# Kernel optimization log

Measured on AMD Instinct MI355X. Metric: run time of the kernel, lower is better.

The kernel has to match this reference:

```python
import jax, jax.numpy as jnp
import numpy as np
from jax import lax

EPS = 1e-5      # InstanceNorm2d default eps
SLOPE = 0.2     # LeakyReLU negative slope
K = 3           # kernel size
PAD = 1


def _conv(x, w, pad=PAD):
    # x: [B,C,H,W], w: [O,I,K,K], stride 1
    return lax.conv_general_dilated(x, w, (1, 1), [(pad, pad), (pad, pad)],
                                    dimension_numbers=('NCHW', 'OIHW', 'NCHW'))


def _instance_norm(x, gamma, beta):
    mu = jnp.mean(x, (2, 3), keepdims=True)
    var = jnp.mean((x - mu) ** 2, (2, 3), keepdims=True)
    xn = (x - mu) * lax.rsqrt(var + EPS)
    return xn * gamma[None, :, None, None] + beta[None, :, None, None]


def _lrelu(x):
    return jnp.where(x >= 0, x, SLOPE * x)


def _deform_conv(x, w_off, b_off, w_def):
    # DCNv2: offsets+mask predicted by a 3x3 conv, then modulated bilinear sampling.
    B, C, H, W = x.shape
    om = _conv(x, w_off) + b_off[None, :, None, None]       # [B, 3*K*K, H, W]
    o1, o2, m = jnp.split(om, 3, axis=1)                    # each [B, K*K, H, W]
    off = jnp.concatenate([o1, o2], axis=1)                 # [B, 2*K*K, H, W]
    dy = off[:, 0::2]                                       # [B, K*K, H, W] y-offsets
    dx = off[:, 1::2]                                       # [B, K*K, H, W] x-offsets
    mask = jax.nn.sigmoid(m)                                # [B, K*K, H, W]

    ky = jnp.repeat(jnp.arange(K), K).astype(x.dtype)       # tap row index per k
    kx = jnp.tile(jnp.arange(K), K).astype(x.dtype)         # tap col index per k
    py = dy + jnp.arange(H, dtype=x.dtype)[None, None, :, None] - PAD + ky[None, :, None, None]
    px = dx + jnp.arange(W, dtype=x.dtype)[None, None, None, :] - PAD + kx[None, :, None, None]

    y0 = jnp.floor(py); x0 = jnp.floor(px)
    ly = py - y0; lx = px - x0
    y0i = y0.astype(jnp.int32); x0i = x0.astype(jnp.int32)

    xf = x.reshape(B, C, H * W)

    def gather(iy, ix):
        valid = ((iy >= 0) & (iy < H) & (ix >= 0) & (ix < W)).astype(x.dtype)
        idx = jnp.clip(iy, 0, H - 1) * W + jnp.clip(ix, 0, W - 1)
        v = jax.vmap(lambda f, i: jnp.take(f, i, axis=-1))(xf, idx)  # [B,C,K*K,H,W]
        return v * valid[:, None]

    samp = (gather(y0i, x0i)         * ((1 - ly) * (1 - lx))[:, None]
          + gather(y0i, x0i + 1)     * ((1 - ly) * lx)[:, None]
          + gather(y0i + 1, x0i)     * (ly * (1 - lx))[:, None]
          + gather(y0i + 1, x0i + 1) * (ly * lx)[:, None])          # [B,C,K*K,H,W]

    wk = w_def.reshape(w_def.shape[0], C, K * K)            # [O,C,K*K]
    return jnp.einsum('ock,bckhw,bkhw->bohw', wk, samp, mask)


def setup_inputs() -> dict:
    key = jax.random.key(0)
    ks = jax.random.split(key, 10)
    B, C, H, W = 4, 128, 96, 96
    x = jax.random.normal(ks[0], (B, C, H, W), jnp.float32)
    g1 = 1.0 + 0.05 * jax.random.normal(ks[1], (C,), jnp.float32)
    b1 = 0.05 * jax.random.normal(ks[2], (C,), jnp.float32)
    g2 = 1.0 + 0.05 * jax.random.normal(ks[3], (C,), jnp.float32)
    b2 = 0.05 * jax.random.normal(ks[4], (C,), jnp.float32)
    w1 = jax.random.normal(ks[5], (C, C, K, K), jnp.float32) * 0.03
    bc1 = 0.01 * jax.random.normal(ks[6], (C,), jnp.float32)
    # offset/mask conv: zero-init in the original; use small random values so the
    # irregular bilinear-sampling path is actually exercised.
    w_off = jax.random.normal(ks[7], (3 * K * K, C, K, K), jnp.float32) * 0.01
    b_off = 0.01 * jax.random.normal(ks[8], (3 * K * K,), jnp.float32)
    w_def = jax.random.normal(ks[9], (C, C, K, K), jnp.float32) * 0.03  # DeformConv has bias=None
    return {"x": x, "g1": g1, "b1": b1, "g2": g2, "b2": b2,
            "w1": w1, "bc1": bc1, "w_off": w_off, "b_off": b_off, "w_def": w_def}


def reference(x, g1, b1, g2, b2, w1, bc1, w_off, b_off, w_def):
    h = _lrelu(_instance_norm(x, g1, b1))
    h = _conv(h, w1) + bc1[None, :, None, None]
    h = _lrelu(_instance_norm(h, g2, b2))
    h = _deform_conv(h, w_off, b_off, w_def)
    return h + x
```

## Files before the change

### kernel.cpp

```cpp
#include <hip/hip_runtime.h>
#include <hip/hip_fp16.h>
#include <math.h>

#define HWN 9216
#define HD 96
#define WD 96

typedef _Float16 h8v __attribute__((ext_vector_type(8)));
typedef float f16x16 __attribute__((ext_vector_type(16)));

__device__ __forceinline__ ushort f2h(float f) {
  return __half_as_ushort(__float2half(f));
}
__device__ __forceinline__ __half2 u2h(unsigned u) {
  return __builtin_bit_cast(__half2, u);
}
__device__ __forceinline__ unsigned h2u(__half2 h) {
  return __builtin_bit_cast(unsigned, h);
}
__device__ __forceinline__ h8v u4h(uint4 v) {
  return __builtin_bit_cast(h8v, v);
}
__device__ __forceinline__ f16x16 mfma32(h8v a, h8v b, f16x16 c) {
  return __builtin_amdgcn_mfma_f32_32x32x16_f16(a, b, c, 0, 0, 0);
}
__device__ __forceinline__ __half2 pkmax2(__half2 a, __half2 b) {
  unsigned r;
  asm("v_pk_max_f16 %0, %1, %2" : "=v"(r) : "v"(h2u(a)), "v"(h2u(b)));
  return u2h(r);
}
__device__ __forceinline__ __half2 lrelu2(__half2 v, __half2 c02) {
  return pkmax2(v, __hmul2(v, c02));
}

__global__ __launch_bounds__(256) void packxt_kernel(
    const float* __restrict__ w1, const float* __restrict__ wdef,
    const float* __restrict__ woff, const float* __restrict__ x,
    ushort* __restrict__ w1p, ushort* __restrict__ wdp, ushort* __restrict__ wofp,
    unsigned* __restrict__ xh, float* __restrict__ partS, float* __restrict__ partQ) {
  __shared__ float tl[128][97];
  int bid = blockIdx.x;
  int t = threadIdx.x;
  if (bid < 162) {
    int i = bid * 256 + t;
    const float* src;
    ushort* dst;
    int CT, CO_real, fi;
    if (i < 18432) { src = w1; dst = w1p; CT = 4; CO_real = 128; fi = i; }
    else if (i < 36864) { src = wdef; dst = wdp; CT = 4; CO_real = 128; fi = i - 18432; }
    else { src = woff; dst = wofp; CT = 1; CO_real = 27; fi = i - 36864; }
    int lane = fi & 63;
    int j = fi >> 6;
    int ks = j & 7; j >>= 3;
    int ct = j % CT;
    int kk = j / CT;
    int co = ct * 32 + (lane & 31);
    int c0 = ks * 16 + (lane >> 5) * 8;
    ushort fr[8];
#pragma unroll
    for (int e = 0; e < 8; ++e) {
      float v = 0.f;
      if (co < CO_real) v = src[(size_t)(co * 128 + c0 + e) * 9 + kk];
      fr[e] = f2h(v);
    }
    uint4 o4;
    o4.x = (unsigned)fr[0] | ((unsigned)fr[1] << 16);
    o4.y = (unsigned)fr[2] | ((unsigned)fr[3] << 16);
    o4.z = (unsigned)fr[4] | ((unsigned)fr[5] << 16);
    o4.w = (unsigned)fr[6] | ((unsigned)fr[7] << 16);
    *(uint4*)(dst + (size_t)fi * 8) = o4;
    return;
  }
  int xb = bid - 162;
  int b = xb / 96, y = xb % 96;
  const float* sbase = x + (size_t)b * 128 * HWN + y * WD;
  for (int i = t; i < 12288; i += 256) {
    int c = i / 96, xx = i - c * 96;
    tl[c][xx] = sbase[(size_t)c * HWN + xx];
  }
  __syncthreads();
  {
    int c = t >> 1, half = t & 1;
    float S = 0.f, Q = 0.f;
    for (int j = 0; j < 48; ++j) {
      float v = tl[c][half * 48 + j];
      S += v;
      Q += v * v;
    }
    S += __shfl_xor(S, 1, 64);
    Q += __shfl_xor(Q, 1, 64);
    if (half == 0) {
      partS[((size_t)(b * 96 + y)) * 128 + c] = S;
      partQ[((size_t)(b * 96 + y)) * 128 + c] = Q;
    }
  }
  unsigned* dbase = xh + (size_t)(b * 96 + y) * 96 * 64;
  for (int i = t; i < 6144; i += 256) {
    int xx = i >> 6, c2 = i & 63;
    unsigned lo = f2h(tl[2 * c2][xx]);
    unsigned hi = f2h(tl[2 * c2 + 1][xx]);
    dbase[xx * 64 + c2] = lo | (hi << 16);
  }
}

__global__ __launch_bounds__(64) void finalize_kernel(
    const float* __restrict__ partS, const float* __restrict__ partQ,
    const float* __restrict__ gamma, const float* __restrict__ beta,
    float* __restrict__ sa_, float* __restrict__ sb_, int ntiles) {
  int bc = blockIdx.x;
  int b = bc >> 7, c = bc & 127;
  float S = 0.f, Q = 0.f;
  for (int tl = threadIdx.x; tl < ntiles; tl += 64) {
    S += partS[((size_t)b * ntiles + tl) * 128 + c];
    Q += partQ[((size_t)b * ntiles + tl) * 128 + c];
  }
#pragma unroll
  for (int off = 32; off > 0; off >>= 1) {
    S += __shfl_down(S, off, 64);
    Q += __shfl_down(Q, off, 64);
  }
  if (threadIdx.x == 0) {
    float mu = S / (float)HWN;
    float var = Q / (float)HWN - mu * mu;
    float rs = rsqrtf(var + 1e-5f);
    float a = rs * gamma[c];
    sa_[bc] = a;
    sb_[bc] = beta[c] - mu * a;
  }
}

__global__ __launch_bounds__(256) void stats2_kernel(
    const ushort* __restrict__ hBh, float* __restrict__ partS,
    float* __restrict__ partQ) {
  int tile = blockIdx.x;
  int b = blockIdx.y;
  int t = threadIdx.x;
  int cc = t & 15, pp = t >> 4;
  int wid = t >> 6, lane = t & 63;
  const ushort* base = hBh + ((size_t)b * HWN + tile * 144) * 128 + cc * 8;
  float S[8], Q[8];
#pragma unroll
  for (int e = 0; e < 8; ++e) { S[e] = 0.f; Q[e] = 0.f; }
  for (int i = 0; i < 9; ++i) {
    int pix = i * 16 + pp;
    uint4 v = *(const uint4*)(base + (size_t)pix * 128);
    unsigned ar[4] = {v.x, v.y, v.z, v.w};
#pragma unroll
    for (int j = 0; j < 4; ++j) {
      float2 f = __half22float2(u2h(ar[j]));
      S[2 * j] += f.x; Q[2 * j] += f.x * f.x;
      S[2 * j + 1] += f.y; Q[2 * j + 1] += f.y * f.y;
    }
  }
#pragma unroll
  for (int e = 0; e < 8; ++e) {
    S[e] += __shfl_xor(S[e], 16, 64); Q[e] += __shfl_xor(Q[e], 16, 64);
    S[e] += __shfl_xor(S[e], 32, 64); Q[e] += __shfl_xor(Q[e], 32, 64);
  }
  __shared__ float red[2][4][16][8];
  if (lane < 16) {
#pragma unroll
    for (int e = 0; e < 8; ++e) { red[0][wid][lane][e] = S[e]; red[1][wid][lane][e] = Q[e]; }
  }
  __syncthreads();
  if (t < 16) {
#pragma unroll
    for (int e = 0; e < 8; ++e) {
      float s = red[0][0][t][e] + red[0][1][t][e] + red[0][2][t][e] + red[0][3][t][e];
      float q = red[1][0][t][e] + red[1][1][t][e] + red[1][2][t][e] + red[1][3][t][e];
      partS[((size_t)b * 64 + tile) * 128 + t * 8 + e] = s;
      partQ[((size_t)b * 64 + tile) * 128 + t * 8 + e] = q;
    }
  }
}

__global__ __launch_bounds__(512) void conv1_mfma(
    const ushort* __restrict__ inp, const float* __restrict__ sa_,
    const float* __restrict__ sb_, const ushort* __restrict__ wp,
    const float* __restrict__ bias, ushort* __restrict__ outh) {
  __shared__ ushort halo[100 * 128];
  __shared__ __half2 sah[64], sbh[64];
  int b = blockIdx.y;
  int tile = blockIdx.x;
  int Y0 = (tile / 12) * 8, X0 = (tile % 12) * 8;
  int t = threadIdx.x;
  int lane = t & 63, w = t >> 6;
  if (t < 64) {
    sah[t] = __floats2half2_rn(sa_[b * 128 + 2 * t], sa_[b * 128 + 2 * t + 1]);
    sbh[t] = __floats2half2_rn(sb_[b * 128 + 2 * t], sb_[b * 128 + 2 * t + 1]);
  }
  __syncthreads();
  const __half2 c02 = __float2half2_rn(0.2f);
  const ushort* ib = inp + (size_t)b * HWN * 128;
  for (int i = t; i < 400; i += 512) {
    int r = i >> 2, q = i & 3;
    int gy = Y0 - 1 + r / 10, gx = X0 - 1 + r % 10;
    bool inb = ((unsigned)gy < 96u) && ((unsigned)gx < 96u);
    const uint4* gp4 = (const uint4*)(ib + (size_t)(gy * 96 + gx) * 128 + q * 32);
#pragma unroll
    for (int cc = 0; cc < 4; ++cc) {
      uint4 v = make_uint4(0, 0, 0, 0);
      if (inb) {
        uint4 g = gp4[cc];
        unsigned ar[4] = {g.x, g.y, g.z, g.w};
        int c2b = (q * 4 + cc) * 4;
#pragma unroll
        for (int j = 0; j < 4; ++j) {
          __half2 hv = __hfma2(u2h(ar[j]), sah[c2b + j], sbh[c2b + j]);
          hv = lrelu2(hv, c02);
          ar[j] = h2u(hv);
        }
        v.x = ar[0]; v.y = ar[1]; v.z = ar[2]; v.w = ar[3];
      }
      int ch = (q * 4 + cc) ^ (r & 7);
      *(uint4*)&halo[r * 128 + ch * 8] = v;
    }
  }
  __syncthreads();

  int ct = w >> 1, pt = w & 1;
  int pl = lane & 31, kh = lane >> 5;
  int p = pt * 32 + pl;
  f16x16 acc = (f16x16)(0.f);

  uint4 Acur[8], Anxt[8];
#pragma unroll
  for (int ks = 0; ks < 8; ++ks)
    Acur[ks] = *(const uint4*)(wp + (size_t)((0 * 4 + ct) * 8 + ks) * 512 + lane * 8);

  for (int kk = 0; kk < 9; ++kk) {
    if (kk < 8) {
#pragma unroll
      for (int ks = 0; ks < 8; ++ks)
        Anxt[ks] = *(const uint4*)(wp + (size_t)(((kk + 1) * 4 + ct) * 8 + ks) * 512 + lane * 8);
    }
    int ky = kk / 3, kx = kk % 3;
    int r = ((p >> 3) + ky) * 10 + (p & 7) + kx;
    __builtin_amdgcn_s_setprio(1);
#pragma unroll
    for (int ks = 0; ks < 8; ++ks) {
      int u = (ks * 2 + kh) ^ (r & 7);
      h8v bf = *(const h8v*)&halo[r * 128 + u * 8];
      acc = mfma32(u4h(Acur[ks]), bf, acc);
    }
    __builtin_amdgcn_s_setprio(0);
    if (kk < 8) {
#pragma unroll
      for (int ks = 0; ks < 8; ++ks) Acur[ks] = Anxt[ks];
    }
  }
  int gp = (Y0 + (p >> 3)) * 96 + X0 + (p & 7);
#pragma unroll
  for (int g = 0; g < 4; ++g) {
    int ch0 = ct * 32 + 4 * kh + 8 * g;
    float v0 = acc[4 * g + 0] + bias[ch0 + 0];
    float v1 = acc[4 * g + 1] + bias[ch0 + 1];
    float v2 = acc[4 * g + 2] + bias[ch0 + 2];
    float v3 = acc[4 * g + 3] + bias[ch0 + 3];
    uint2 o;
    o.x = (unsigned)f2h(v0) | ((unsigned)f2h(v1) << 16);
    o.y = (unsigned)f2h(v2) | ((unsigned)f2h(v3) << 16);
    *(uint2*)&outh[((size_t)b * HWN + gp) * 128 + ch0] = o;
  }
}

__device__ __forceinline__ uint4 gaffine(const ushort* hb, int pix, int cc,
                                         const __half2* sa2v, const __half2* sb2v,
                                         __half2 c02) {
  uint4 g = *(const uint4*)(hb + (size_t)pix * 128 + cc * 8);
  unsigned ar[4] = {g.x, g.y, g.z, g.w};
#pragma unroll
  for (int j = 0; j < 4; ++j) {
    __half2 hv = __hfma2(u2h(ar[j]), sa2v[j], sb2v[j]);
    hv = lrelu2(hv, c02);
    ar[j] = h2u(hv);
  }
  return make_uint4(ar[0], ar[1], ar[2], ar[3]);
}

__global__ __launch_bounds__(256) void deform_fused(
    const ushort* __restrict__ h2n, const float* __restrict__ sa_,
    const float* __restrict__ sb_, const ushort* __restrict__ wofp,
    const float* __restrict__ boff, const ushort* __restrict__ wdp,
    const float* __restrict__ x, float* __restrict__ out) {
  __shared__ __align__(16) ushort halo[96 * 128];
  __shared__ __align__(16) ushort S[2][32 * 128];
  __shared__ __align__(16) ushort4 idxs[9][32];
  __shared__ __align__(16) ushort4 wgtc[9][32];
  __shared__ __half2 sah[64], sbh[64];
  float* pf = (float*)S;
  int bid = blockIdx.x;
  int swz = (bid & 7) * 144 + (bid >> 3);
  int b = swz / 288;
  int tile = swz % 288;
  int Y0 = (tile / 12) * 4, X0 = (tile % 12) * 8;
  int t = threadIdx.x;
  int lane = t & 63, w = t >> 6;
  const ushort* hb = h2n + (size_t)b * HWN * 128;
  if (t < 64) {
    sah[t] = __floats2half2_rn(sa_[b * 128 + 2 * t], sa_[b * 128 + 2 * t + 1]);
    sbh[t] = __floats2half2_rn(sb_[b * 128 + 2 * t], sb_[b * 128 + 2 * t + 1]);
  }
  __syncthreads();
  const __half2 c02 = __float2half2_rn(0.2f);

  for (int i = t; i < 1536; i += 256) {
    int pix = i >> 4, u = i & 15;
    int gy = Y0 - 2 + pix / 12, gx = X0 - 2 + pix % 12;
    uint4 v = make_uint4(0, 0, 0, 0);
    if (((unsigned)gy < 96u) && ((unsigned)gx < 96u)) {
      uint4 g = *(const uint4*)(hb + (size_t)(gy * 96 + gx) * 128 + u * 8);
      unsigned ar[4] = {g.x, g.y, g.z, g.w};
#pragma unroll
      for (int j = 0; j < 4; ++j) {
        __half2 hv = __hfma2(u2h(ar[j]), sah[u * 4 + j], sbh[u * 4 + j]);
        hv = lrelu2(hv, c02);
        ar[j] = h2u(hv);
      }
      v.x = ar[0]; v.y = ar[1]; v.z = ar[2]; v.w = ar[3];
    }
    *(uint4*)&halo[pix * 128 + ((u ^ (pix & 15)) * 8)] = v;
  }
  __syncthreads();

  {
    int pl = lane & 31, kh = lane >> 5;
    int p = pl;
    f16x16 accm = (f16x16)(0.f);
    for (int kk = w; kk < 9; kk += 4) {
      int ky = kk / 3, kx = kk % 3;
      int hp = (1 + (p >> 3) + ky) * 12 + 1 + (p & 7) + kx;
#pragma unroll
      for (int ks = 0; ks < 8; ++ks) {
        uint4 a = *(const uint4*)(wofp + (size_t)(kk * 8 + ks) * 512 + lane * 8);
        int u = (ks * 2 + kh) ^ (hp & 15);
        h8v bf = *(const h8v*)&halo[hp * 128 + u * 8];
        accm = mfma32(u4h(a), bf, accm);
      }
    }
#pragma unroll
    for (int reg = 0; reg < 16; ++reg) {
      int co = 4 * kh + (reg & 3) + 8 * (reg >> 2);
      pf[(w * 32 + co) * 32 + p] = accm[reg];
    }
  }
  __syncthreads();

  for (int i = t; i < 288; i += 256) {
    int k = i >> 5, p = i & 31;
    int yy = Y0 + (p >> 3), xx = X0 + (p & 7);
    int cdy = 2 * k, cdx = 2 * k + 1, cm = 18 + k;
    float dy = pf[(0 * 32 + cdy) * 32 + p] + pf[(1 * 32 + cdy) * 32 + p] +
               pf[(2 * 32 + cdy) * 32 + p] + pf[(3 * 32 + cdy) * 32 + p] + boff[cdy];
    float dx = pf[(0 * 32 + cdx) * 32 + p] + pf[(1 * 32 + cdx) * 32 + p] +
               pf[(2 * 32 + cdx) * 32 + p] + pf[(3 * 32 + cdx) * 32 + p] + boff[cdx];
    float mv = pf[(0 * 32 + cm) * 32 + p] + pf[(1 * 32 + cm) * 32 + p] +
               pf[(2 * 32 + cm) * 32 + p] + pf[(3 * 32 + cm) * 32 + p] + boff[cm];
    float mask = 1.0f / (1.0f + expf(-mv));
    float py = dy + (float)(yy - 1 + (k / 3));
    float px = dx + (float)(xx - 1 + (k % 3));
    float fy = floorf(py), fx = floorf(px);
    float lyf = py - fy, lxf = px - fx;
    int y0 = (int)fy, x0 = (int)fx;
    int y1 = y0 + 1, x1 = x0 + 1;
    bool vy0 = (y0 >= 0) && (y0 < HD);
    bool vy1 = (y1 >= 0) && (y1 < HD);
    bool vx0 = (x0 >= 0) && (x0 < WD);
    bool vx1 = (x1 >= 0) && (x1 < WD);
    int y0c = min(max(y0, 0), HD - 1), y1c = min(max(y1, 0), HD - 1);
    int x0c = min(max(x0, 0), WD - 1), x1c = min(max(x1, 0), WD - 1);
    float w0 = (1.f - lyf) * (1.f - lxf) * ((vy0 && vx0) ? mask : 0.f);
    float w1v = (1.f - lyf) * lxf * ((vy0 && vx1) ? mask : 0.f);
    float w2 = lyf * (1.f - lxf) * ((vy1 && vx0) ? mask : 0.f);
    float w3 = lyf * lxf * ((vy1 && vx1) ? mask : 0.f);
    bool inh = (y0c >= Y0 - 2) && (y1c <= Y0 + 5) && (x0c >= X0 - 2) && (x1c <= X0 + 9);
    ushort4 sidx;
    if (inh) {
      int sy0 = y0c - (Y0 - 2), sy1 = y1c - (Y0 - 2);
      int sx0 = x0c - (X0 - 2), sx1 = x1c - (X0 - 2);
      sidx.x = (ushort)(sy0 * 12 + sx0);
      sidx.y = (ushort)(sy0 * 12 + sx1);
      sidx.z = (ushort)(sy1 * 12 + sx0);
      sidx.w = (ushort)(sy1 * 12 + sx1);
    } else {
      sidx.x = (ushort)((y0c * WD + x0c) | 0x8000);
      sidx.y = (ushort)(y0c * WD + x1c);
      sidx.z = (ushort)(y1c * WD + x0c);
      sidx.w = (ushort)(y1c * WD + x1c);
    }
    idxs[k][p] = sidx;
    ushort4 wc;
    wc.x = f2h(w0); wc.y = f2h(w1v); wc.z = f2h(w2); wc.w = f2h(w3);
    wgtc[k][p] = wc;
  }
  __syncthreads();

  int cc = t & 15;
  int pp = t >> 4;
  int ct = w;
  int pl = lane & 31, kh = lane >> 5;
  int pg = pl;
  f16x16 acc = (f16x16)(0.f);
  __half2 sa2v[4], sb2v[4];
#pragma unroll
  for (int j = 0; j < 4; ++j) { sa2v[j] = sah[cc * 4 + j]; sb2v[j] = sbh[cc * 4 + j]; }

  int gp = (Y0 + (pg >> 3)) * 96 + X0 + (pg & 7);
  float xr[16];
#pragma unroll
  for (int reg = 0; reg < 16; ++reg) {
    int co = ct * 32 + 4 * kh + (reg & 3) + 8 * (reg >> 2);
    xr[reg] = x[(size_t)(b * 128 + co) * HWN + gp];
  }

  uint4 AW[8];
  for (int k = 0; k < 9; ++k) {
    const ushort* wk = wdp + (size_t)k * 16384;
#pragma unroll
    for (int ks = 0; ks < 8; ++ks)
      AW[ks] = *(const uint4*)(wk + (size_t)(ct * 8 + ks) * 512 + lane * 8);
    ushort* Sb_w = S[k & 1];
#pragma unroll
    for (int i2 = 0; i2 < 2; ++i2) {
      int p = pp + 16 * i2;
      ushort4 sidx = idxs[k][p];
      ushort4 wc = wgtc[k][p];
      uint4 C0, C1, C2, C3;
      if (sidx.x & 0x8000u) {
        C0 = gaffine(hb, sidx.x & 0x7fff, cc, sa2v, sb2v, c02);
        C1 = gaffine(hb, sidx.y, cc, sa2v, sb2v, c02);
        C2 = gaffine(hb, sidx.z, cc, sa2v, sb2v, c02);
        C3 = gaffine(hb, sidx.w, cc, sa2v, sb2v, c02);
      } else {
        C0 = *(const uint4*)&halo[sidx.x * 128 + ((cc ^ (sidx.x & 15)) * 8)];
        C1 = *(const uint4*)&halo[sidx.y * 128 + ((cc ^ (sidx.y & 15)) * 8)];
        C2 = *(const uint4*)&halo[sidx.z * 128 + ((cc ^ (sidx.z & 15)) * 8)];
        C3 = *(const uint4*)&halo[sidx.w * 128 + ((cc ^ (sidx.w & 15)) * 8)];
      }
      __half2 a0 = u2h((unsigned)wc.x * 0x10001u);
      __half2 a1 = u2h((unsigned)wc.y * 0x10001u);
      __half2 a2 = u2h((unsigned)wc.z * 0x10001u);
      __half2 a3 = u2h((unsigned)wc.w * 0x10001u);
      __half2 s0 = __hmul2(u2h(C0.x), a0);
      __half2 s1 = __hmul2(u2h(C0.y), a0);
      __half2 s2 = __hmul2(u2h(C0.z), a0);
      __half2 s3 = __hmul2(u2h(C0.w), a0);
      s0 = __hfma2(u2h(C1.x), a1, s0); s1 = __hfma2(u2h(C1.y), a1, s1);
      s2 = __hfma2(u2h(C1.z), a1, s2); s3 = __hfma2(u2h(C1.w), a1, s3);
      s0 = __hfma2(u2h(C2.x), a2, s0); s1 = __hfma2(u2h(C2.y), a2, s1);
      s2 = __hfma2(u2h(C2.z), a2, s2); s3 = __hfma2(u2h(C2.w), a2, s3);
      s0 = __hfma2(u2h(C3.x), a3, s0); s1 = __hfma2(u2h(C3.y), a3, s1);
      s2 = __hfma2(u2h(C3.z), a3, s2); s3 = __hfma2(u2h(C3.w), a3, s3);
      uint4 o4;
      o4.x = h2u(s0); o4.y = h2u(s1); o4.z = h2u(s2); o4.w = h2u(s3);
      *(uint4*)&Sb_w[p * 128 + ((cc ^ (p & 15)) * 8)] = o4;
    }
    asm volatile("s_waitcnt lgkmcnt(0)" ::: "memory");
    __builtin_amdgcn_s_barrier();
    const ushort* Sb = S[k & 1];
    __builtin_amdgcn_s_setprio(1);
#pragma unroll
    for (int ks = 0; ks < 8; ++ks) {
      int u = (ks * 2 + kh) ^ (pg & 15);
      h8v bf = *(const h8v*)&Sb[pg * 128 + u * 8];
      acc = mfma32(u4h(AW[ks]), bf, acc);
    }
    __builtin_amdgcn_s_setprio(0);
  }
#pragma unroll
  for (int reg = 0; reg < 16; ++reg) {
    int co = ct * 32 + 4 * kh + (reg & 3) + 8 * (reg >> 2);
    size_t oi = (size_t)(b * 128 + co) * HWN + gp;
    out[oi] = acc[reg] + xr[reg];
  }
}

extern "C" void kernel_launch(void* const* d_in, const int* in_sizes, int n_in,
                              void* d_out, int out_size, void* d_ws, size_t ws_size,
                              hipStream_t stream) {
  const float* x = (const float*)d_in[0];
  const float* g1 = (const float*)d_in[1];
  const float* b1 = (const float*)d_in[2];
  const float* g2 = (const float*)d_in[3];
  const float* b2 = (const float*)d_in[4];
  const float* w1 = (const float*)d_in[5];
  const float* bc1 = (const float*)d_in[6];
  const float* w_off = (const float*)d_in[7];
  const float* b_off = (const float*)d_in[8];
  const float* w_def = (const float*)d_in[9];
  float* out = (float*)d_out;
  float* ws = (float*)d_ws;

  ushort* w1p = (ushort*)ws;
  ushort* wofp = (ushort*)(ws + 73728);
  ushort* wdp = (ushort*)(ws + 92160);
  float* sa1 = ws + 165888;
  float* sb1 = ws + 166400;
  float* sa2 = ws + 166912;
  float* sb2 = ws + 167424;
  float* partS1 = ws + 167936;
  float* partQ1 = ws + 217088;
  float* partS2 = ws + 266240;
  float* partQ2 = ws + 299008;
  ushort* xh = (ushort*)(ws + 331776);
  ushort* hBh = (ushort*)(ws + 2691072);

  packxt_kernel<<<546, 256, 0, stream>>>(w1, w_def, w_off, x, w1p, wdp, wofp,
                                         (unsigned*)xh, partS1, partQ1);
  finalize_kernel<<<512, 64, 0, stream>>>(partS1, partQ1, g1, b1, sa1, sb1, 96);
  conv1_mfma<<<dim3(144, 4), 512, 0, stream>>>(xh, sa1, sb1, w1p, bc1, hBh);
  stats2_kernel<<<dim3(64, 4), 256, 0, stream>>>(hBh, partS2, partQ2);
  finalize_kernel<<<512, 64, 0, stream>>>(partS2, partQ2, g2, b2, sa2, sb2, 64);
  deform_fused<<<dim3(1152), 256, 0, stream>>>(hBh, sa2, sb2, wofp, b_off, wdp, x, out);
}
```

Before: 81.90 us.

## Fold instance-norm finalize into consumer kernels and vectorize x tile loads

Removes the two finalize_kernel launches by having each block of conv1_mfma and deform_fused reduce the per-tile partial sums itself and compute the norm scale and shift in shared memory. Also switches the x-tile load in packxt to float4 reads. This cuts two kernel launches and their dependency gaps. In exchange every block redundantly re-reads the partial sums (96 or 64 rows by 128 channels, twice) and pays extra barriers at kernel start.

```diff
diff --git a/kernel.cpp b/kernel.cpp
--- a/kernel.cpp
+++ b/kernel.cpp
@@ -74,9 +74,13 @@
   int xb = bid - 162;
   int b = xb / 96, y = xb % 96;
   const float* sbase = x + (size_t)b * 128 * HWN + y * WD;
-  for (int i = t; i < 12288; i += 256) {
-    int c = i / 96, xx = i - c * 96;
-    tl[c][xx] = sbase[(size_t)c * HWN + xx];
+  for (int i = t; i < 3072; i += 256) {
+    int c = i / 24, j = i - c * 24;
+    const float4 v = *(const float4*)(sbase + (size_t)c * HWN + j * 4);
+    tl[c][j * 4 + 0] = v.x;
+    tl[c][j * 4 + 1] = v.y;
+    tl[c][j * 4 + 2] = v.z;
+    tl[c][j * 4 + 3] = v.w;
   }
   __syncthreads();
   {
@@ -100,32 +104,6 @@
     unsigned lo = f2h(tl[2 * c2][xx]);
     unsigned hi = f2h(tl[2 * c2 + 1][xx]);
     dbase[xx * 64 + c2] = lo | (hi << 16);
-  }
-}
-
-__global__ __launch_bounds__(64) void finalize_kernel(
-    const float* __restrict__ partS, const float* __restrict__ partQ,
-    const float* __restrict__ gamma, const float* __restrict__ beta,
-    float* __restrict__ sa_, float* __restrict__ sb_, int ntiles) {
-  int bc = blockIdx.x;
-  int b = bc >> 7, c = bc & 127;
-  float S = 0.f, Q = 0.f;
-  for (int tl = threadIdx.x; tl < ntiles; tl += 64) {
-    S += partS[((size_t)b * ntiles + tl) * 128 + c];
-    Q += partQ[((size_t)b * ntiles + tl) * 128 + c];
-  }
-#pragma unroll
-  for (int off = 32; off > 0; off >>= 1) {
-    S += __shfl_down(S, off, 64);
-    Q += __shfl_down(Q, off, 64);
-  }
-  if (threadIdx.x == 0) {
-    float mu = S / (float)HWN;
-    float var = Q / (float)HWN - mu * mu;
-    float rs = rsqrtf(var + 1e-5f);
-    float a = rs * gamma[c];
-    sa_[bc] = a;
-    sb_[bc] = beta[c] - mu * a;
   }
 }
 
@@ -175,8 +153,9 @@
 }
 
 __global__ __launch_bounds__(512) void conv1_mfma(
-    const ushort* __restrict__ inp, const float* __restrict__ sa_,
-    const float* __restrict__ sb_, const ushort* __restrict__ wp,
+    const ushort* __restrict__ inp, const float* __restrict__ partS1,
+    const float* __restrict__ partQ1, const float* __restrict__ g1v,
+    const float* __restrict__ b1v, const ushort* __restrict__ wp,
     const float* __restrict__ bias, ushort* __restrict__ outh) {
   __shared__ ushort halo[100 * 128];
   __shared__ __half2 sah[64], sbh[64];
@@ -185,9 +164,34 @@
   int Y0 = (tile / 12) * 8, X0 = (tile % 12) * 8;
   int t = threadIdx.x;
   int lane = t & 63, w = t >> 6;
+  float* fredp = (float*)halo;
+  float* saf = fredp + 1024;
+  float* sbf = saf + 128;
+  {
+    int c = t & 127, g = t >> 7;
+    float S = 0.f, Q = 0.f;
+    for (int r = g * 24; r < g * 24 + 24; ++r) {
+      S += partS1[((size_t)(b * 96 + r)) * 128 + c];
+      Q += partQ1[((size_t)(b * 96 + r)) * 128 + c];
+    }
+    fredp[(0 * 4 + g) * 128 + c] = S;
+    fredp[(1 * 4 + g) * 128 + c] = Q;
+  }
+  __syncthreads();
+  if (t < 128) {
+    float S = fredp[0 * 128 + t] + fredp[1 * 128 + t] + fredp[2 * 128 + t] + fredp[3 * 128 + t];
+    float Q = fredp[4 * 128 + t] + fredp[5 * 128 + t] + fredp[6 * 128 + t] + fredp[7 * 128 + t];
+    float mu = S / (float)HWN;
+    float var = Q / (float)HWN - mu * mu;
+    float rs = rsqrtf(var + 1e-5f);
+    float a = rs * g1v[t];
+    saf[t] = a;
+    sbf[t] = b1v[t] - mu * a;
+  }
+  __syncthreads();
   if (t < 64) {
-    sah[t] = __floats2half2_rn(sa_[b * 128 + 2 * t], sa_[b * 128 + 2 * t + 1]);
-    sbh[t] = __floats2half2_rn(sb_[b * 128 + 2 * t], sb_[b * 128 + 2 * t + 1]);
+    sah[t] = __floats2half2_rn(saf[2 * t], saf[2 * t + 1]);
+    sbh[t] = __floats2half2_rn(sbf[2 * t], sbf[2 * t + 1]);
   }
   __syncthreads();
   const __half2 c02 = __float2half2_rn(0.2f);
@@ -279,8 +283,9 @@
 }
 
 __global__ __launch_bounds__(256) void deform_fused(
-    const ushort* __restrict__ h2n, const float* __restrict__ sa_,
-    const float* __restrict__ sb_, const ushort* __restrict__ wofp,
+    const ushort* __restrict__ h2n, const float* __restrict__ partS2,
+    const float* __restrict__ partQ2, const float* __restrict__ g2v,
+    const float* __restrict__ b2v, const ushort* __restrict__ wofp,
     const float* __restrict__ boff, const ushort* __restrict__ wdp,
     const float* __restrict__ x, float* __restrict__ out) {
   __shared__ __align__(16) ushort halo[96 * 128];
@@ -297,11 +302,38 @@
   int t = threadIdx.x;
   int lane = t & 63, w = t >> 6;
   const ushort* hb = h2n + (size_t)b * HWN * 128;
-  if (t < 64) {
-    sah[t] = __floats2half2_rn(sa_[b * 128 + 2 * t], sa_[b * 128 + 2 * t + 1]);
-    sbh[t] = __floats2half2_rn(sb_[b * 128 + 2 * t], sb_[b * 128 + 2 * t + 1]);
-  }
-  __syncthreads();
+  {
+    float* fredp = (float*)halo;
+    float* saf = fredp + 512;
+    float* sbf = saf + 128;
+    {
+      int c = t & 127, g = t >> 7;
+      float Sv = 0.f, Qv = 0.f;
+      for (int r = g * 32; r < g * 32 + 32; ++r) {
+        Sv += partS2[((size_t)b * 64 + r) * 128 + c];
+        Qv += partQ2[((size_t)b * 64 + r) * 128 + c];
+      }
+      fredp[(0 * 2 + g) * 128 + c] = Sv;
+      fredp[(1 * 2 + g) * 128 + c] = Qv;
+    }
+    __syncthreads();
+    if (t < 128) {
+      float Sv = fredp[0 * 128 + t] + fredp[1 * 128 + t];
+      float Qv = fredp[2 * 128 + t] + fredp[3 * 128 + t];
+      float mu = Sv / (float)HWN;
+      float var = Qv / (float)HWN - mu * mu;
+      float rs = rsqrtf(var + 1e-5f);
+      float a = rs * g2v[t];
+      saf[t] = a;
+      sbf[t] = b2v[t] - mu * a;
+    }
+    __syncthreads();
+    if (t < 64) {
+      sah[t] = __floats2half2_rn(saf[2 * t], saf[2 * t + 1]);
+      sbh[t] = __floats2half2_rn(sbf[2 * t], sbf[2 * t + 1]);
+    }
+    __syncthreads();
+  }
   const __half2 c02 = __float2half2_rn(0.2f);
 
   for (int i = t; i < 1536; i += 256) {
@@ -494,22 +526,17 @@
   ushort* w1p = (ushort*)ws;
   ushort* wofp = (ushort*)(ws + 73728);
   ushort* wdp = (ushort*)(ws + 92160);
-  float* sa1 = ws + 165888;
-  float* sb1 = ws + 166400;
-  float* sa2 = ws + 166912;
-  float* sb2 = ws + 167424;
-  float* partS1 = ws + 167936;
-  float* partQ1 = ws + 217088;
-  float* partS2 = ws + 266240;
-  float* partQ2 = ws + 299008;
-  ushort* xh = (ushort*)(ws + 331776);
-  ushort* hBh = (ushort*)(ws + 2691072);
+  float* partS1 = ws + 165888;
+  float* partQ1 = ws + 215040;
+  float* partS2 = ws + 264192;
+  float* partQ2 = ws + 296960;
+  ushort* xh = (ushort*)(ws + 329728);
+  ushort* hBh = (ushort*)(ws + 2689024);
 
   packxt_kernel<<<546, 256, 0, stream>>>(w1, w_def, w_off, x, w1p, wdp, wofp,
                                          (unsigned*)xh, partS1, partQ1);
-  finalize_kernel<<<512, 64, 0, stream>>>(partS1, partQ1, g1, b1, sa1, sb1, 96);
-  conv1_mfma<<<dim3(144, 4), 512, 0, stream>>>(xh, sa1, sb1, w1p, bc1, hBh);
+  conv1_mfma<<<dim3(144, 4), 512, 0, stream>>>(xh, partS1, partQ1, g1, b1, w1p, bc1, hBh);
   stats2_kernel<<<dim3(64, 4), 256, 0, stream>>>(hBh, partS2, partQ2);
-  finalize_kernel<<<512, 64, 0, stream>>>(partS2, partQ2, g2, b2, sa2, sb2, 64);
-  deform_fused<<<dim3(1152), 256, 0, stream>>>(hBh, sa2, sb2, wofp, b_off, wdp, x, out);
-}
+  deform_fused<<<dim3(1152), 256, 0, stream>>>(hBh, partS2, partQ2, g2, b2, wofp, b_off,
+                                               wdp, x, out);
+}
```

Result: slower. 99.33 us (+21.3%).
